# Kernel optimization log

Measured on AMD Instinct MI355X. Metric: run time of the kernel, lower is better.

## Reference

```python
import jax, jax.numpy as jnp
import numpy as np

DIM = 1024
NUM_HEADS = 16
REL_DIM = 32
B, N = 8, 512


def setup_inputs() -> dict:
    key = jax.random.key(0)
    ks = jax.random.split(key, 8)
    s = 0.02
    return {
        "x": jax.random.normal(ks[0], (B, N, DIM), dtype=jnp.float32),
        "rel_bias": jax.random.normal(ks[1], (B, N, N, REL_DIM), dtype=jnp.float32),
        # torch nn.Linear convention: weight (out_features, in_features)
        "W_qkv": jax.random.normal(ks[2], (3 * DIM, DIM), dtype=jnp.float32) * s,
        "b_qkv": jax.random.normal(ks[3], (3 * DIM,), dtype=jnp.float32) * s,
        "W_rel": jax.random.normal(ks[4], (NUM_HEADS, REL_DIM), dtype=jnp.float32) * s,
        "b_rel": jax.random.normal(ks[5], (NUM_HEADS,), dtype=jnp.float32) * s,
        "W_out": jax.random.normal(ks[6], (DIM, DIM), dtype=jnp.float32) * s,
        "b_out": jax.random.normal(ks[7], (DIM,), dtype=jnp.float32) * s,
    }


def reference(x, rel_bias, W_qkv, b_qkv, W_rel, b_rel, W_out, b_out):
    Bx, Nx, D = x.shape
    H = NUM_HEADS
    hd = D // H
    # QKV projection: (B,N,3D) -> (B,N,3,H,hd)
    qkv = (x @ W_qkv.T + b_qkv).reshape(Bx, Nx, 3, H, hd)
    q, k, v = qkv[:, :, 0], qkv[:, :, 1], qkv[:, :, 2]
    scale = hd ** -0.5
    attn = jnp.einsum('bnhd,bmhd->bhnm', q, k) * scale
    # per-pair relative bias projected to heads: (B,N,N,H) -> (B,H,N,N)
    rel = (rel_bias @ W_rel.T + b_rel).transpose(0, 3, 1, 2)
    attn = jax.nn.softmax(attn + rel, axis=-1)
    out = jnp.einsum('bhnm,bmhd->bnhd', attn, v).reshape(Bx, Nx, D)
    return out @ W_out.T + b_out
```

## Files before the change

### kernel.cpp

```cpp
#include <hip/hip_runtime.h>

typedef unsigned short u16;
typedef unsigned int u32;
typedef __attribute__((ext_vector_type(8))) __bf16 bf16x8;
typedef __attribute__((ext_vector_type(4))) float f32x4;

union U8 {
  bf16x8 b;
  uint2 u2[2];
  uint4 u4;
  u32 w[4];
  u16 us[8];
};

__device__ __forceinline__ u16 f2bf(float f) {
  u32 x = __float_as_uint(f);
  x += 0x7FFFu + ((x >> 16) & 1u);
  return (u16)(x >> 16);
}
__device__ __forceinline__ float bf2f(u16 u) {
  return __uint_as_float(((u32)u) << 16);
}
__device__ __forceinline__ u32 cvtpk(float lo, float hi) {
  u32 r;
  asm("v_cvt_pk_bf16_f32 %0, %1, %2" : "=v"(r) : "v"(lo), "v"(hi));
  return r;
}

#define GLOAD16(gp, lp)                                                          \
  __builtin_amdgcn_global_load_lds(                                              \
      (const __attribute__((address_space(1))) unsigned int*)(const void*)(gp),  \
      (__attribute__((address_space(3))) unsigned int*)(void*)(lp), 16, 0, 0)

__global__ void k_convert_all(const float* __restrict__ x, const float* __restrict__ wq,
                              const float* __restrict__ wo, u16* __restrict__ xb,
                              u16* __restrict__ wqb, u16* __restrict__ wob) {
  const int NX = 1048576, NQ = 786432, NO = 262144;
  int idx = blockIdx.x * blockDim.x + threadIdx.x;
  int stride = gridDim.x * blockDim.x;
  for (int i = idx; i < NX + NQ + NO; i += stride) {
    const float4* s;
    ushort4* d;
    int k;
    if (i < NX) { s = (const float4*)x; d = (ushort4*)xb; k = i; }
    else if (i < NX + NQ) { s = (const float4*)wq; d = (ushort4*)wqb; k = i - NX; }
    else { s = (const float4*)wo; d = (ushort4*)wob; k = i - NX - NQ; }
    float4 v = s[k];
    ushort4 o;
    o.x = f2bf(v.x); o.y = f2bf(v.y); o.z = f2bf(v.z); o.w = f2bf(v.w);
    d[k] = o;
  }
}

__global__ __launch_bounds__(256) void k_rel(const float* __restrict__ rb,
                                             const float* __restrict__ Wr,
                                             const float* __restrict__ br,
                                             u16* __restrict__ out) {
  const int t = threadIdx.x;
  const int lane = t & 63, c2 = t >> 6;
  const int i16 = lane & 15, g4 = lane >> 4;
  const int mt = blockIdx.x, nt = blockIdx.y, b = blockIdx.z;

  U8 wb;
  {
    const float* wp = Wr + i16 * 32 + 8 * g4;
    float4 w0 = *(const float4*)wp;
    float4 w1 = *(const float4*)(wp + 4);
    wb.w[0] = cvtpk(w0.x, w0.y);
    wb.w[1] = cvtpk(w0.z, w0.w);
    wb.w[2] = cvtpk(w1.x, w1.y);
    wb.w[3] = cvtpk(w1.z, w1.w);
  }
  const float bias = br[i16];

  const int m = mt * 64 + c2 * 16 + i16;
  const float* rbase = rb + ((size_t)(b * 512 + nt * 16) * 512 + m) * 32 + 8 * g4;
  const size_t base =
      ((((size_t)(b * 16 + i16)) * 32 + nt) * 8 + mt) * 1024 + c2 * 256 + g4 * 16;

#pragma unroll
  for (int gp = 0; gp < 4; ++gp) {
    f32x4 accv[4];
#pragma unroll
    for (int k = 0; k < 4; ++k) {
      int ni = 4 * gp + k;
      float4 a0 = *(const float4*)(rbase + (size_t)ni * 16384);
      float4 a1 = *(const float4*)(rbase + (size_t)ni * 16384 + 4);
      U8 af;
      af.w[0] = cvtpk(a0.x, a0.y);
      af.w[1] = cvtpk(a0.z, a0.w);
      af.w[2] = cvtpk(a1.x, a1.y);
      af.w[3] = cvtpk(a1.z, a1.w);
      f32x4 ci = {bias, bias, bias, bias};
      accv[k] = __builtin_amdgcn_mfma_f32_16x16x32_bf16(af.b, wb.b, ci, 0, 0, 0);
    }
    u32 wd[8];
#pragma unroll
    for (int w = 0; w < 8; ++w) {
      int jj = w >> 1, jlo = 2 * (w & 1);
      wd[w] = cvtpk(accv[jlo][jj], accv[jlo + 1][jj]);
    }
    uint4 s0 = {wd[0], wd[1], wd[2], wd[3]};
    uint4 s1 = {wd[4], wd[5], wd[6], wd[7]};
    *(uint4*)(out + base + gp * 64) = s0;
    *(uint4*)(out + base + gp * 64 + 8) = s1;
  }
}

__global__ __launch_bounds__(256) void k_gemm_qkv(const u16* __restrict__ A,
                                                  const u16* __restrict__ Bm,
                                                  const float* __restrict__ bias,
                                                  u16* __restrict__ Qo, u16* __restrict__ Ko,
                                                  u16* __restrict__ Vo) {
  const int K = 1024;
  __shared__ u16 Al[128 * 64];
  __shared__ u16 Bl[128 * 64];
  const int t = threadIdx.x;
  const int lane = t & 63, wid = t >> 6;
  const int g = lane >> 4, i16 = lane & 15;
  const int wm = wid >> 1, wn = wid & 1;
  const int bm = blockIdx.y, bn = blockIdx.x;

  f32x4 zero = {0.f, 0.f, 0.f, 0.f};
  f32x4 acc[4][4];
#pragma unroll
  for (int mi = 0; mi < 4; ++mi)
#pragma unroll
    for (int ni = 0; ni < 4; ++ni) acc[mi][ni] = zero;

  int srow[4], sgc[4];
#pragma unroll
  for (int i = 0; i < 4; ++i) {
    int ch = wid * 256 + i * 64 + lane;
    int r = ch >> 3, cs = ch & 7;
    srow[i] = r;
    sgc[i] = cs ^ (r & 7);
  }

  for (int k0 = 0; k0 < K; k0 += 64) {
    __syncthreads();
#pragma unroll
    for (int i = 0; i < 4; ++i) {
      const u16* ga = A + (size_t)(bm * 128 + srow[i]) * K + k0 + sgc[i] * 8;
      const u16* gb = Bm + (size_t)(bn * 128 + srow[i]) * K + k0 + sgc[i] * 8;
      GLOAD16(ga, Al + (size_t)(wid * 256 + i * 64) * 8);
      GLOAD16(gb, Bl + (size_t)(wid * 256 + i * 64) * 8);
    }
    __syncthreads();

#pragma unroll
    for (int kk = 0; kk < 2; ++kk) {
      U8 af[4], bfr[4];
#pragma unroll
      for (int mi = 0; mi < 4; ++mi) {
        int row = wm * 64 + mi * 16 + i16;
        int ch = (g + 4 * kk) ^ (row & 7);
        af[mi].u4 = *(const uint4*)(Al + row * 64 + ch * 8);
      }
#pragma unroll
      for (int ni = 0; ni < 4; ++ni) {
        int row = wn * 64 + ni * 16 + i16;
        int ch = (g + 4 * kk) ^ (row & 7);
        bfr[ni].u4 = *(const uint4*)(Bl + row * 64 + ch * 8);
      }
#pragma unroll
      for (int mi = 0; mi < 4; ++mi)
#pragma unroll
        for (int ni = 0; ni < 4; ++ni)
          acc[mi][ni] = __builtin_amdgcn_mfma_f32_16x16x32_bf16(af[mi].b, bfr[ni].b,
                                                                acc[mi][ni], 0, 0, 0);
    }
  }

#pragma unroll
  for (int mi = 0; mi < 4; ++mi) {
#pragma unroll
    for (int ni = 0; ni < 4; ++ni) {
      int col = bn * 128 + wn * 64 + ni * 16 + i16;
      int row0 = bm * 128 + wm * 64 + mi * 16 + 4 * g;
      float bia = bias[col];
      int tt = col >> 10;
      int h = (col >> 6) & 15;
      int d = col & 63;
      int b = row0 >> 9;
      int n0 = row0 & 511;
      if (tt < 2) {
        u16* dst = (tt == 0) ? Qo : Ko;
#pragma unroll
        for (int j = 0; j < 4; ++j)
          dst[((size_t)(b * 16 + h) * 512 + n0 + j) * 64 + d] = f2bf(acc[mi][ni][j] + bia);
      } else {
        uint2 w;
        w.x = cvtpk(acc[mi][ni][0] + bia, acc[mi][ni][1] + bia);
        w.y = cvtpk(acc[mi][ni][2] + bia, acc[mi][ni][3] + bia);
        *(uint2*)(Vo + ((size_t)(b * 16 + h) * 64 + d) * 512 + n0) = w;
      }
    }
  }
}

__global__ __launch_bounds__(256) void k_gemm_out(const u16* __restrict__ A,
                                                  const u16* __restrict__ Bm,
                                                  const float* __restrict__ bias,
                                                  float* __restrict__ Co) {
  const int K = 1024;
  __shared__ u16 Al[128 * 64];
  __shared__ u16 Bl[128 * 64];
  const int t = threadIdx.x;
  const int lane = t & 63, wid = t >> 6;
  const int g = lane >> 4, i16 = lane & 15;
  const int wm = wid >> 1, wn = wid & 1;
  const int bm = blockIdx.y, bn = blockIdx.x;

  f32x4 zero = {0.f, 0.f, 0.f, 0.f};
  f32x4 acc[4][4];
#pragma unroll
  for (int mi = 0; mi < 4; ++mi)
#pragma unroll
    for (int ni = 0; ni < 4; ++ni) acc[mi][ni] = zero;

  int srow[4], sgc[4];
#pragma unroll
  for (int i = 0; i < 4; ++i) {
    int ch = wid * 256 + i * 64 + lane;
    int r = ch >> 3, cs = ch & 7;
    srow[i] = r;
    sgc[i] = cs ^ (r & 7);
  }

  for (int k0 = 0; k0 < K; k0 += 64) {
    __syncthreads();
#pragma unroll
    for (int i = 0; i < 4; ++i) {
      GLOAD16(A + (size_t)(bm * 128 + srow[i]) * K + k0 + sgc[i] * 8,
              Al + (size_t)(wid * 256 + i * 64) * 8);
      GLOAD16(Bm + (size_t)(bn * 128 + srow[i]) * K + k0 + sgc[i] * 8,
              Bl + (size_t)(wid * 256 + i * 64) * 8);
    }
    __syncthreads();

#pragma unroll
    for (int kk = 0; kk < 2; ++kk) {
      U8 af[4], bfr[4];
#pragma unroll
      for (int mi = 0; mi < 4; ++mi) {
        int row = wm * 64 + mi * 16 + i16;
        int ch = (g + 4 * kk) ^ (row & 7);
        af[mi].u4 = *(const uint4*)(Al + row * 64 + ch * 8);
      }
#pragma unroll
      for (int ni = 0; ni < 4; ++ni) {
        int row = wn * 64 + ni * 16 + i16;
        int ch = (g + 4 * kk) ^ (row & 7);
        bfr[ni].u4 = *(const uint4*)(Bl + row * 64 + ch * 8);
      }
#pragma unroll
      for (int mi = 0; mi < 4; ++mi)
#pragma unroll
        for (int ni = 0; ni < 4; ++ni)
          acc[mi][ni] = __builtin_amdgcn_mfma_f32_16x16x32_bf16(af[mi].b, bfr[ni].b,
                                                                acc[mi][ni], 0, 0, 0);
    }
  }

#pragma unroll
  for (int mi = 0; mi < 4; ++mi) {
#pragma unroll
    for (int ni = 0; ni < 4; ++ni) {
      int col = bn * 128 + wn * 64 + ni * 16 + i16;
      int row0 = bm * 128 + wm * 64 + mi * 16 + 4 * g;
      float bia = bias[col];
#pragma unroll
      for (int j = 0; j < 4; ++j)
        Co[(size_t)(row0 + j) * 1024 + col] = acc[mi][ni][j] + bia;
    }
  }
}

__global__ __launch_bounds__(256) void k_attn(const u16* __restrict__ Q,
                                              const u16* __restrict__ Kb,
                                              const u16* __restrict__ Vtb,
                                              const u16* __restrict__ Rel,
                                              u16* __restrict__ Out) {
  __shared__ u16 Kl[2][64 * 64];
  __shared__ u16 Vl[2][64 * 64];
  __shared__ u16 Pl[4][16 * 68];

  const int qt = blockIdx.x, h = blockIdx.y, b = blockIdx.z;
  const int t = threadIdx.x, lane = t & 63, wid = t >> 6;
  const int g = lane >> 4, i16 = lane & 15;
  const size_t bh = (size_t)(b * 16 + h);

  const u16* Qg = Q + (bh * 512 + qt * 64 + wid * 16 + i16) * 64;
  U8 qf[2];
  qf[0].u4 = *(const uint4*)(Qg + 8 * g);
  qf[1].u4 = *(const uint4*)(Qg + 8 * g + 32);

  float m_run[4], l_run[4];
  f32x4 zero = {0.f, 0.f, 0.f, 0.f};
  f32x4 acc[4];
#pragma unroll
  for (int c = 0; c < 4; ++c) acc[c] = zero;
#pragma unroll
  for (int j = 0; j < 4; ++j) { m_run[j] = -1e30f; l_run[j] = 0.f; }

  int srow[2], sgc[2];
#pragma unroll
  for (int i = 0; i < 2; ++i) {
    int ch = wid * 128 + i * 64 + lane;
    int r = ch >> 3, cs = ch & 7;
    srow[i] = r;
    sgc[i] = cs ^ (r & 7);
  }

  const u16* Kg0 = Kb + bh * 512 * 64;
  const u16* Vg0 = Vtb + bh * 64 * 512;
  const u16* Rg = Rel + ((bh * 32 + qt * 4 + wid) * 8) * 1024 + lane * 4;

#define STAGE(buf, m0)                                                                  \
  do {                                                                                  \
    _Pragma("unroll") for (int i = 0; i < 2; ++i) {                                     \
      GLOAD16(Kg0 + (size_t)((m0) + srow[i]) * 64 + sgc[i] * 8,                         \
              &Kl[buf][(size_t)(wid * 128 + i * 64) * 8]);                              \
      GLOAD16(Vg0 + (size_t)srow[i] * 512 + (m0) + sgc[i] * 8,                          \
              &Vl[buf][(size_t)(wid * 128 + i * 64) * 8]);                              \
    }                                                                                   \
  } while (0)

  STAGE(0, 0);
  __syncthreads();

  for (int it = 0; it < 8; ++it) {
    const int buf = it & 1;
    if (it < 7) STAGE(buf ^ 1, it * 64 + 64);

    uint2 rl[4];
#pragma unroll
    for (int c = 0; c < 4; ++c) rl[c] = *(const uint2*)(Rg + it * 1024 + c * 256);

    f32x4 s[4];
#pragma unroll
    for (int c = 0; c < 4; ++c) s[c] = zero;
    __builtin_amdgcn_s_setprio(1);
#pragma unroll
    for (int c = 0; c < 4; ++c) {
#pragma unroll
      for (int kk = 0; kk < 2; ++kk) {
        int row = c * 16 + i16;
        int ch = (g + 4 * kk) ^ (row & 7);
        U8 kf;
        kf.u4 = *(const uint4*)(&Kl[buf][row * 64 + ch * 8]);
        s[c] = __builtin_amdgcn_mfma_f32_16x16x32_bf16(qf[kk].b, kf.b, s[c], 0, 0, 0);
      }
    }
    __builtin_amdgcn_s_setprio(0);

#pragma unroll
    for (int c = 0; c < 4; ++c) {
      const u16* rc = (const u16*)&rl[c];
#pragma unroll
      for (int j = 0; j < 4; ++j) s[c][j] = s[c][j] * 0.125f + bf2f(rc[j]);
    }
    float fac[4];
#pragma unroll
    for (int j = 0; j < 4; ++j) {
      float pm = fmaxf(fmaxf(s[0][j], s[1][j]), fmaxf(s[2][j], s[3][j]));
      pm = fmaxf(pm, __shfl_xor(pm, 1));
      pm = fmaxf(pm, __shfl_xor(pm, 2));
      pm = fmaxf(pm, __shfl_xor(pm, 4));
      pm = fmaxf(pm, __shfl_xor(pm, 8));
      float mnew = fmaxf(m_run[j], pm);
      fac[j] = __expf(m_run[j] - mnew);
      m_run[j] = mnew;
    }
#pragma unroll
    for (int c = 0; c < 4; ++c)
#pragma unroll
      for (int j = 0; j < 4; ++j) s[c][j] = __expf(s[c][j] - m_run[j]);
#pragma unroll
    for (int j = 0; j < 4; ++j) {
      float rs = s[0][j] + s[1][j] + s[2][j] + s[3][j];
      rs += __shfl_xor(rs, 1);
      rs += __shfl_xor(rs, 2);
      rs += __shfl_xor(rs, 4);
      rs += __shfl_xor(rs, 8);
      l_run[j] = l_run[j] * fac[j] + rs;
    }
#pragma unroll
    for (int c = 0; c < 4; ++c)
#pragma unroll
      for (int j = 0; j < 4; ++j) acc[c][j] *= fac[j];

    u16* Pw = Pl[wid];
#pragma unroll
    for (int c = 0; c < 4; ++c)
#pragma unroll
      for (int j = 0; j < 4; ++j)
        Pw[(4 * g + j) * 68 + c * 16 + i16] = f2bf(s[c][j]);
    __syncthreads();

    U8 pf[2];
#pragma unroll
    for (int kk = 0; kk < 2; ++kk) {
      const u16* p = Pl[wid] + i16 * 68 + 8 * g + 32 * kk;
      pf[kk].u2[0] = *(const uint2*)p;
      pf[kk].u2[1] = *(const uint2*)(p + 4);
    }
    __builtin_amdgcn_s_setprio(1);
#pragma unroll
    for (int c = 0; c < 4; ++c) {
#pragma unroll
      for (int kk = 0; kk < 2; ++kk) {
        int row = c * 16 + i16;
        int ch = (g + 4 * kk) ^ (row & 7);
        U8 vf;
        vf.u4 = *(const uint4*)(&Vl[buf][row * 64 + ch * 8]);
        acc[c] = __builtin_amdgcn_mfma_f32_16x16x32_bf16(pf[kk].b, vf.b, acc[c], 0, 0, 0);
      }
    }
    __builtin_amdgcn_s_setprio(0);
    __syncthreads();
  }
#undef STAGE

#pragma unroll
  for (int c = 0; c < 4; ++c) {
#pragma unroll
    for (int j = 0; j < 4; ++j) {
      int n = qt * 64 + wid * 16 + 4 * g + j;
      float v = acc[c][j] / l_run[j];
      Out[((size_t)b * 512 + n) * 1024 + h * 64 + c * 16 + i16] = f2bf(v);
    }
  }
}

extern "C" void kernel_launch(void* const* d_in, const int* in_sizes, int n_in,
                              void* d_out, int out_size, void* d_ws, size_t ws_size,
                              hipStream_t stream) {
  const float* x = (const float*)d_in[0];
  const float* rel_bias = (const float*)d_in[1];
  const float* W_qkv = (const float*)d_in[2];
  const float* b_qkv = (const float*)d_in[3];
  const float* W_rel = (const float*)d_in[4];
  const float* b_rel = (const float*)d_in[5];
  const float* W_out = (const float*)d_in[6];
  const float* b_out = (const float*)d_in[7];
  float* out = (float*)d_out;

  char* ws = (char*)d_ws;
  u16* x_bf    = (u16*)(ws);
  u16* wqkv_bf = (u16*)(ws + 8388608);
  u16* wout_bf = (u16*)(ws + 14680064);
  u16* Qw      = (u16*)(ws + 16777216);
  u16* Kw      = (u16*)(ws + 25165824);
  u16* Vt      = (u16*)(ws + 33554432);
  u16* relb    = (u16*)(ws + 41943040);
  u16* attno   = (u16*)(ws + 109051904);

  k_convert_all<<<2048, 256, 0, stream>>>(x, W_qkv, W_out, x_bf, wqkv_bf, wout_bf);

  k_rel<<<dim3(8, 32, 8), 256, 0, stream>>>(rel_bias, W_rel, b_rel, relb);

  k_gemm_qkv<<<dim3(24, 32), 256, 0, stream>>>(x_bf, wqkv_bf, b_qkv, Qw, Kw, Vt);

  k_attn<<<dim3(8, 16, 8), 256, 0, stream>>>(Qw, Kw, Vt, relb, attno);

  k_gemm_out<<<dim3(8, 32), 256, 0, stream>>>(attno, wout_bf, b_out, out);
}
```

Measured before the change: 202.4 us.

## Fuse rel-bias projection and QKV GEMM into one interleaved launch

Merges the relative-bias projection kernel and the QKV GEMM into a single launch. Block indices are interleaved so every group of 35 blocks holds 3 compute-bound GEMM tiles and 32 memory-bound rel-bias blocks, letting the two overlap on the same CUs. The rel-bias path also drops MFMA and computes each pair's 16 head outputs with scalar FP32 FMAs, one thread per (n,m) pair. The cost is that the rel blocks reserve the GEMM's shared memory they never use, which may limit occupancy, and the scalar path uses more ALU work and stores that are less coalesced.

Result: no change. 205.3 us (+1.4%).

```diff
diff --git a/kernel.cpp b/kernel.cpp
--- a/kernel.cpp
+++ b/kernel.cpp
@@ -52,149 +52,127 @@
   }
 }
 
-__global__ __launch_bounds__(256) void k_rel(const float* __restrict__ rb,
-                                             const float* __restrict__ Wr,
-                                             const float* __restrict__ br,
-                                             u16* __restrict__ out) {
-  const int t = threadIdx.x;
-  const int lane = t & 63, c2 = t >> 6;
-  const int i16 = lane & 15, g4 = lane >> 4;
-  const int mt = blockIdx.x, nt = blockIdx.y, b = blockIdx.z;
-
-  U8 wb;
-  {
-    const float* wp = Wr + i16 * 32 + 8 * g4;
-    float4 w0 = *(const float4*)wp;
-    float4 w1 = *(const float4*)(wp + 4);
-    wb.w[0] = cvtpk(w0.x, w0.y);
-    wb.w[1] = cvtpk(w0.z, w0.w);
-    wb.w[2] = cvtpk(w1.x, w1.y);
-    wb.w[3] = cvtpk(w1.z, w1.w);
-  }
-  const float bias = br[i16];
-
-  const int m = mt * 64 + c2 * 16 + i16;
-  const float* rbase = rb + ((size_t)(b * 512 + nt * 16) * 512 + m) * 32 + 8 * g4;
-  const size_t base =
-      ((((size_t)(b * 16 + i16)) * 32 + nt) * 8 + mt) * 1024 + c2 * 256 + g4 * 16;
-
-#pragma unroll
-  for (int gp = 0; gp < 4; ++gp) {
-    f32x4 accv[4];
-#pragma unroll
-    for (int k = 0; k < 4; ++k) {
-      int ni = 4 * gp + k;
-      float4 a0 = *(const float4*)(rbase + (size_t)ni * 16384);
-      float4 a1 = *(const float4*)(rbase + (size_t)ni * 16384 + 4);
-      U8 af;
-      af.w[0] = cvtpk(a0.x, a0.y);
-      af.w[1] = cvtpk(a0.z, a0.w);
-      af.w[2] = cvtpk(a1.x, a1.y);
-      af.w[3] = cvtpk(a1.z, a1.w);
-      f32x4 ci = {bias, bias, bias, bias};
-      accv[k] = __builtin_amdgcn_mfma_f32_16x16x32_bf16(af.b, wb.b, ci, 0, 0, 0);
-    }
-    u32 wd[8];
-#pragma unroll
-    for (int w = 0; w < 8; ++w) {
-      int jj = w >> 1, jlo = 2 * (w & 1);
-      wd[w] = cvtpk(accv[jlo][jj], accv[jlo + 1][jj]);
-    }
-    uint4 s0 = {wd[0], wd[1], wd[2], wd[3]};
-    uint4 s1 = {wd[4], wd[5], wd[6], wd[7]};
-    *(uint4*)(out + base + gp * 64) = s0;
-    *(uint4*)(out + base + gp * 64 + 8) = s1;
-  }
-}
-
-__global__ __launch_bounds__(256) void k_gemm_qkv(const u16* __restrict__ A,
-                                                  const u16* __restrict__ Bm,
-                                                  const float* __restrict__ bias,
-                                                  u16* __restrict__ Qo, u16* __restrict__ Ko,
-                                                  u16* __restrict__ Vo) {
-  const int K = 1024;
+__global__ __launch_bounds__(256) void k_fused_rel_qkv(
+    const float* __restrict__ rb, const float* __restrict__ Wr, const float* __restrict__ br,
+    u16* __restrict__ relout, const u16* __restrict__ A, const u16* __restrict__ Bm,
+    const float* __restrict__ bias, u16* __restrict__ Qo, u16* __restrict__ Ko,
+    u16* __restrict__ Vo) {
   __shared__ u16 Al[128 * 64];
   __shared__ u16 Bl[128 * 64];
+
+  const int blk = blockIdx.x;
   const int t = threadIdx.x;
-  const int lane = t & 63, wid = t >> 6;
-  const int g = lane >> 4, i16 = lane & 15;
-  const int wm = wid >> 1, wn = wid & 1;
-  const int bm = blockIdx.y, bn = blockIdx.x;
-
-  f32x4 zero = {0.f, 0.f, 0.f, 0.f};
-  f32x4 acc[4][4];
-#pragma unroll
-  for (int mi = 0; mi < 4; ++mi)
-#pragma unroll
-    for (int ni = 0; ni < 4; ++ni) acc[mi][ni] = zero;
-
-  int srow[4], sgc[4];
-#pragma unroll
-  for (int i = 0; i < 4; ++i) {
-    int ch = wid * 256 + i * 64 + lane;
-    int r = ch >> 3, cs = ch & 7;
-    srow[i] = r;
-    sgc[i] = cs ^ (r & 7);
-  }
-
-  for (int k0 = 0; k0 < K; k0 += 64) {
-    __syncthreads();
+  const int grp = blk / 35, sl = blk % 35;
+
+  if (sl < 3) {
+    const int gid = grp * 3 + sl;
+    const int bn = gid % 24, bm = gid / 24;
+    const int K = 1024;
+    const int lane = t & 63, wid = t >> 6;
+    const int g = lane >> 4, i16 = lane & 15;
+    const int wm = wid >> 1, wn = wid & 1;
+
+    f32x4 zero = {0.f, 0.f, 0.f, 0.f};
+    f32x4 acc[4][4];
+#pragma unroll
+    for (int mi = 0; mi < 4; ++mi)
+#pragma unroll
+      for (int ni = 0; ni < 4; ++ni) acc[mi][ni] = zero;
+
+    int srow[4], sgc[4];
 #pragma unroll
     for (int i = 0; i < 4; ++i) {
-      const u16* ga = A + (size_t)(bm * 128 + srow[i]) * K + k0 + sgc[i] * 8;
-      const u16* gb = Bm + (size_t)(bn * 128 + srow[i]) * K + k0 + sgc[i] * 8;
-      GLOAD16(ga, Al + (size_t)(wid * 256 + i * 64) * 8);
-      GLOAD16(gb, Bl + (size_t)(wid * 256 + i * 64) * 8);
-    }
-    __syncthreads();
-
-#pragma unroll
-    for (int kk = 0; kk < 2; ++kk) {
-      U8 af[4], bfr[4];
-#pragma unroll
-      for (int mi = 0; mi < 4; ++mi) {
-        int row = wm * 64 + mi * 16 + i16;
-        int ch = (g + 4 * kk) ^ (row & 7);
-        af[mi].u4 = *(const uint4*)(Al + row * 64 + ch * 8);
-      }
+      int ch = wid * 256 + i * 64 + lane;
+      int r = ch >> 3, cs = ch & 7;
+      srow[i] = r;
+      sgc[i] = cs ^ (r & 7);
+    }
+
+    for (int k0 = 0; k0 < K; k0 += 64) {
+      __syncthreads();
+#pragma unroll
+      for (int i = 0; i < 4; ++i) {
+        const u16* ga = A + (size_t)(bm * 128 + srow[i]) * K + k0 + sgc[i] * 8;
+        const u16* gb = Bm + (size_t)(bn * 128 + srow[i]) * K + k0 + sgc[i] * 8;
+        GLOAD16(ga, Al + (size_t)(wid * 256 + i * 64) * 8);
+        GLOAD16(gb, Bl + (size_t)(wid * 256 + i * 64) * 8);
+      }
+      __syncthreads();
+
+#pragma unroll
+      for (int kk = 0; kk < 2; ++kk) {
+        U8 af[4], bfr[4];
+#pragma unroll
+        for (int mi = 0; mi < 4; ++mi) {
+          int row = wm * 64 + mi * 16 + i16;
+          int ch = (g + 4 * kk) ^ (row & 7);
+          af[mi].u4 = *(const uint4*)(Al + row * 64 + ch * 8);
+        }
+#pragma unroll
+        for (int ni = 0; ni < 4; ++ni) {
+          int row = wn * 64 + ni * 16 + i16;
+          int ch = (g + 4 * kk) ^ (row & 7);
+          bfr[ni].u4 = *(const uint4*)(Bl + row * 64 + ch * 8);
+        }
+#pragma unroll
+        for (int mi = 0; mi < 4; ++mi)
+#pragma unroll
+          for (int ni = 0; ni < 4; ++ni)
+            acc[mi][ni] = __builtin_amdgcn_mfma_f32_16x16x32_bf16(af[mi].b, bfr[ni].b,
+                                                                  acc[mi][ni], 0, 0, 0);
+      }
+    }
+
+#pragma unroll
+    for (int mi = 0; mi < 4; ++mi) {
 #pragma unroll
       for (int ni = 0; ni < 4; ++ni) {
-        int row = wn * 64 + ni * 16 + i16;
-        int ch = (g + 4 * kk) ^ (row & 7);
-        bfr[ni].u4 = *(const uint4*)(Bl + row * 64 + ch * 8);
-      }
-#pragma unroll
-      for (int mi = 0; mi < 4; ++mi)
-#pragma unroll
-        for (int ni = 0; ni < 4; ++ni)
-          acc[mi][ni] = __builtin_amdgcn_mfma_f32_16x16x32_bf16(af[mi].b, bfr[ni].b,
-                                                                acc[mi][ni], 0, 0, 0);
-    }
-  }
-
-#pragma unroll
-  for (int mi = 0; mi < 4; ++mi) {
-#pragma unroll
-    for (int ni = 0; ni < 4; ++ni) {
-      int col = bn * 128 + wn * 64 + ni * 16 + i16;
-      int row0 = bm * 128 + wm * 64 + mi * 16 + 4 * g;
-      float bia = bias[col];
-      int tt = col >> 10;
-      int h = (col >> 6) & 15;
-      int d = col & 63;
-      int b = row0 >> 9;
-      int n0 = row0 & 511;
-      if (tt < 2) {
-        u16* dst = (tt == 0) ? Qo : Ko;
-#pragma unroll
-        for (int j = 0; j < 4; ++j)
-          dst[((size_t)(b * 16 + h) * 512 + n0 + j) * 64 + d] = f2bf(acc[mi][ni][j] + bia);
-      } else {
-        uint2 w;
-        w.x = cvtpk(acc[mi][ni][0] + bia, acc[mi][ni][1] + bia);
-        w.y = cvtpk(acc[mi][ni][2] + bia, acc[mi][ni][3] + bia);
-        *(uint2*)(Vo + ((size_t)(b * 16 + h) * 64 + d) * 512 + n0) = w;
-      }
+        int col = bn * 128 + wn * 64 + ni * 16 + i16;
+        int row0 = bm * 128 + wm * 64 + mi * 16 + 4 * g;
+        float bia = bias[col];
+        int tt = col >> 10;
+        int h = (col >> 6) & 15;
+        int d = col & 63;
+        int b = row0 >> 9;
+        int n0 = row0 & 511;
+        if (tt < 2) {
+          u16* dst = (tt == 0) ? Qo : Ko;
+#pragma unroll
+          for (int j = 0; j < 4; ++j)
+            dst[((size_t)(b * 16 + h) * 512 + n0 + j) * 64 + d] = f2bf(acc[mi][ni][j] + bia);
+        } else {
+          uint2 w;
+          w.x = cvtpk(acc[mi][ni][0] + bia, acc[mi][ni][1] + bia);
+          w.y = cvtpk(acc[mi][ni][2] + bia, acc[mi][ni][3] + bia);
+          *(uint2*)(Vo + ((size_t)(b * 16 + h) * 64 + d) * 512 + n0) = w;
+        }
+      }
+    }
+  } else {
+    const int rid = grp * 32 + (sl - 3);
+    const int mt = rid & 7, ntg = (rid >> 3) & 127, b = rid >> 10;
+    const int i16 = t & 15, j = (t >> 4) & 3, c = t >> 6;
+    const int nt = ntg >> 2, g = ntg & 3;
+    const int n = nt * 16 + 4 * g + j;
+    const int m = mt * 64 + c * 16 + i16;
+
+    const float4* rp = (const float4*)(rb + ((size_t)(b * 512 + n) * 512 + m) * 32);
+    float4 r4[8];
+#pragma unroll
+    for (int q = 0; q < 8; ++q) r4[q] = rp[q];
+
+    const size_t obase =
+        (((size_t)(b * 16) * 32 + nt) * 8 + mt) * 1024 + c * 256 + (g * 16 + i16) * 4 + j;
+#pragma unroll
+    for (int h = 0; h < 16; ++h) {
+      float acc = br[h];
+      const float* w = Wr + h * 32;
+#pragma unroll
+      for (int q = 0; q < 8; ++q) {
+        acc += r4[q].x * w[4 * q + 0] + r4[q].y * w[4 * q + 1] +
+               r4[q].z * w[4 * q + 2] + r4[q].w * w[4 * q + 3];
+      }
+      relout[obase + (size_t)h * 262144] = f2bf(acc);
     }
   }
 }
@@ -459,9 +437,8 @@
 
   k_convert_all<<<2048, 256, 0, stream>>>(x, W_qkv, W_out, x_bf, wqkv_bf, wout_bf);
 
-  k_rel<<<dim3(8, 32, 8), 256, 0, stream>>>(rel_bias, W_rel, b_rel, relb);
-
-  k_gemm_qkv<<<dim3(24, 32), 256, 0, stream>>>(x_bf, wqkv_bf, b_qkv, Qw, Kw, Vt);
+  k_fused_rel_qkv<<<8960, 256, 0, stream>>>(rel_bias, W_rel, b_rel, relb, x_bf, wqkv_bf,
+                                            b_qkv, Qw, Kw, Vt);
 
   k_attn<<<dim3(8, 16, 8), 256, 0, stream>>>(Qw, Kw, Vt, relb, attno);
 
```
